# Optimization experiments

Hardware: AMD Instinct MI355X
Metric: run time of the kernel (lower is better)

The kernel has to match this reference:

```python
import jax, jax.numpy as jnp
import numpy as np

N = 50000          # nodes
E = 1_600_000      # edges (avg degree 32)
IN = 128           # in_channels
H = 64             # hidden_channels = middle_channel
OUT = 40           # out_channels
ALPHA = 0.8
NO_GRAD_STEPS = 3  # iter_nums = (4, 1) -> 3 no-grad + 1 grad step
GRAD_STEPS = 1
LN_EPS = 1e-5


def setup_inputs() -> dict:
    key = jax.random.key(0)
    ks = jax.random.split(key, 8)
    x = jax.random.normal(ks[0], (N, IN), jnp.float32)
    edge_index = jax.random.randint(ks[1], (2, E), 0, N, dtype=jnp.int64)
    # per-node symmetric-normalization factor, strictly positive (deg^-1/2-like)
    norm_factor = jax.random.uniform(ks[2], (N, 1), jnp.float32, 0.1, 1.0)
    kaiming = lambda k, shape, fan_in: jax.random.normal(k, shape, jnp.float32) * np.float32(np.sqrt(2.0 / fan_in))
    We = kaiming(ks[3], (H, IN), IN)      # extractor weight
    be = jnp.zeros((H,), jnp.float32)
    W = kaiming(ks[4], (H, H), H)         # Implicit_Func.W (no bias)
    U = kaiming(ks[5], (H, H), H)         # Implicit_Func.U
    bU = jnp.zeros((H,), jnp.float32)
    gamma = jnp.ones((H,), jnp.float32)   # LayerNorm affine
    beta = jnp.zeros((H,), jnp.float32)
    Wlast = jax.random.normal(ks[6], (OUT, H), jnp.float32) * np.float32(np.sqrt(2.0 / (H + OUT)))  # xavier
    blast = jnp.zeros((OUT,), jnp.float32)
    return dict(x=x, edge_index=edge_index, norm_factor=norm_factor,
                We=We, be=be, W=W, U=U, bU=bU, gamma=gamma, beta=beta,
                Wlast=Wlast, blast=blast)


def _layernorm(m, gamma, beta):
    mu = jnp.mean(m, axis=-1, keepdims=True)
    var = jnp.mean((m - mu) ** 2, axis=-1, keepdims=True)
    return gamma * (m - mu) * jax.lax.rsqrt(var + LN_EPS) + beta


def _step(z, xU, nf, row, col, W, gamma, beta):
    # WzUx = norm_factor * (W z + degree * U x)   (xU precomputed as degree*(Ux+b))
    h = nf * (z @ W.T + xU)                       # [N, H]
    m = jnp.tanh(h[row] - h[col])                 # gather-diff + act, [E, H]
    m = _layernorm(m, gamma, beta)
    # scatter_add back to nodes with norm weighting
    a = (jax.ops.segment_sum(m * nf[row], row, num_segments=N)
         - jax.ops.segment_sum(m * nf[col], col, num_segments=N))  # [N, H]
    new_z = -(a @ W)                              # F.linear(a, W.t()) = a @ W
    return ALPHA * new_z + (1.0 - ALPHA) * z


def reference(x, edge_index, norm_factor, We, be, W, U, bU, gamma, beta, Wlast, blast):
    row, col = edge_index[0], edge_index[1]
    xh = x @ We.T + be                            # extractor, [N, H]
    degree = 1.0 / norm_factor
    degree = jnp.where(jnp.isinf(degree), 0.0, degree)
    xU = degree * (xh @ U.T + bU)                 # constant across iterations
    z = jnp.zeros_like(xh)
    for _ in range(NO_GRAD_STEPS):
        z = _step(z, xU, norm_factor, row, col, W, gamma, beta)
    z = jax.lax.stop_gradient(z)
    for _ in range(GRAD_STEPS):
        z = _step(z, xU, norm_factor, row, col, W, gamma, beta)
    z = norm_factor * z + xh                      # rescale + residual
    return z @ Wlast.T + blast                    # linear head, [N, OUT]
```

## Files before the change

kernel.cpp:

```cpp
#include <hip/hip_runtime.h>
#include <hip/hip_bf16.h>

#define NN   50000
#define EE   1600000
#define INC  128
#define HH   64
#define OUTC 40
#define ALPHA 0.8f
#define LN_EPS 1e-5f
#define NB_SCAN 196
#define KTANH 2.8853900817779268f

typedef int v4i_t __attribute__((ext_vector_type(4)));
typedef _Float16 h8 __attribute__((ext_vector_type(8)));
typedef float f32x4 __attribute__((ext_vector_type(4)));

__device__ float llvm_amdgcn_raw_buffer_load_fp32(v4i_t srsrc, int voffset,
                                                  int soffset, int glc_slc)
    __asm("llvm.amdgcn.raw.buffer.load.f32");

__device__ __forceinline__ float rl63(float x) {
    return __int_as_float(__builtin_amdgcn_readlane(__float_as_int(x), 63));
}
#define RLF(X, L) __int_as_float(__builtin_amdgcn_readlane(__float_as_int(X), (L)))

__device__ __forceinline__ float fast_tanh_pre(float xs) {
    float e = __builtin_amdgcn_exp2f(xs);
    float u = __builtin_amdgcn_rcpf(1.0f + e);
    return __builtin_fmaf(-2.0f, u, 1.0f);
}

struct TileAcc { float a0, a1, a2, a3, sc; };

template <bool GUARD>
__device__ __forceinline__ void tile16(
        TileAcc& A, float hn, int nrem,
        float h0, float h1, float h2, float h3,
        float h4, float h5, float h6, float h7,
        float h8v, float h9, float h10, float h11,
        float h12, float h13, float h14, float h15,
        _Float16* tb, int wt, int wlow, int roff0, int roff1, h8 ones) {
    float d0 = fast_tanh_pre(hn - h0);
    float d1 = fast_tanh_pre(hn - h1);
    float d2 = fast_tanh_pre(hn - h2);
    float d3 = fast_tanh_pre(hn - h3);
    float d4 = fast_tanh_pre(hn - h4);
    float d5 = fast_tanh_pre(hn - h5);
    float d6 = fast_tanh_pre(hn - h6);
    float d7 = fast_tanh_pre(hn - h7);
    float d8 = fast_tanh_pre(hn - h8v);
    float d9 = fast_tanh_pre(hn - h9);
    float d10 = fast_tanh_pre(hn - h10);
    float d11 = fast_tanh_pre(hn - h11);
    float d12 = fast_tanh_pre(hn - h12);
    float d13 = fast_tanh_pre(hn - h13);
    float d14 = fast_tanh_pre(hn - h14);
    float d15 = fast_tanh_pre(hn - h15);
    if (GUARD) {
        if (!(0 < nrem))  d0 = 0.f;
        if (!(1 < nrem))  d1 = 0.f;
        if (!(2 < nrem))  d2 = 0.f;
        if (!(3 < nrem))  d3 = 0.f;
        if (!(4 < nrem))  d4 = 0.f;
        if (!(5 < nrem))  d5 = 0.f;
        if (!(6 < nrem))  d6 = 0.f;
        if (!(7 < nrem))  d7 = 0.f;
        if (!(8 < nrem))  d8 = 0.f;
        if (!(9 < nrem))  d9 = 0.f;
        if (!(10 < nrem)) d10 = 0.f;
        if (!(11 < nrem)) d11 = 0.f;
        if (!(12 < nrem)) d12 = 0.f;
        if (!(13 < nrem)) d13 = 0.f;
        if (!(14 < nrem)) d14 = 0.f;
        if (!(15 < nrem)) d15 = 0.f;
    }
#define WRT(E, D)                                                             \
    {                                                                         \
        int ix = ((wt ^ ((E) & 7)) << 3) + wlow + ((E) << 6);                 \
        tb[ix] = (_Float16)(D);                                               \
        tb[ix + 1024] = (_Float16)((D) * (D));                                \
    }
    WRT(0, d0)   WRT(1, d1)   WRT(2, d2)   WRT(3, d3)
    WRT(4, d4)   WRT(5, d5)   WRT(6, d6)   WRT(7, d7)
    WRT(8, d8)   WRT(9, d9)   WRT(10, d10) WRT(11, d11)
    WRT(12, d12) WRT(13, d13) WRT(14, d14) WRT(15, d15)
#undef WRT
    h8 a0 = *(const h8*)(tb + roff0);
    h8 a1 = *(const h8*)(tb + roff1);
    h8 q0 = *(const h8*)(tb + 1024 + roff0);
    h8 q1 = *(const h8*)(tb + 1024 + roff1);
    f32x4 s1 = {0.f, 0.f, 0.f, 0.f}, s2 = {0.f, 0.f, 0.f, 0.f};
    s1 = __builtin_amdgcn_mfma_f32_16x16x32_f16(a0, ones, s1, 0, 0, 0);
    s1 = __builtin_amdgcn_mfma_f32_16x16x32_f16(a1, ones, s1, 0, 0, 0);
    s2 = __builtin_amdgcn_mfma_f32_16x16x32_f16(q0, ones, s2, 0, 0, 0);
    s2 = __builtin_amdgcn_mfma_f32_16x16x32_f16(q1, ones, s2, 0, 0, 0);
    float mu0 = s1[0] * 0.015625f;
    float mu1 = s1[1] * 0.015625f;
    float mu2 = s1[2] * 0.015625f;
    float mu3 = s1[3] * 0.015625f;
    float v0 = __builtin_fmaf(s2[0], 0.015625f, __builtin_fmaf(-mu0, mu0, LN_EPS));
    float v1 = __builtin_fmaf(s2[1], 0.015625f, __builtin_fmaf(-mu1, mu1, LN_EPS));
    float v2 = __builtin_fmaf(s2[2], 0.015625f, __builtin_fmaf(-mu2, mu2, LN_EPS));
    float v3 = __builtin_fmaf(s2[3], 0.015625f, __builtin_fmaf(-mu3, mu3, LN_EPS));
    float rs0 = __frsqrt_rn(v0);
    float rs1 = __frsqrt_rn(v1);
    float rs2 = __frsqrt_rn(v2);
    float rs3 = __frsqrt_rn(v3);
    float cs = __builtin_fmaf(rs0, mu0,
               __builtin_fmaf(rs1, mu1,
               __builtin_fmaf(rs2, mu2, rs3 * mu3)));
    asm volatile(
        "s_nop 1\n\t"
        "v_add_f32_dpp %0, %0, %0 row_bcast:15 row_mask:0xa bank_mask:0xf bound_ctrl:0\n\t"
        "s_nop 1\n\t"
        "v_add_f32_dpp %0, %0, %0 row_bcast:31 row_mask:0xc bank_mask:0xf bound_ctrl:0"
        : "+v"(cs));
    A.sc += rl63(cs);
    A.a0 = __builtin_fmaf(RLF(rs0, 0), d0, A.a0);
    A.a1 = __builtin_fmaf(RLF(rs1, 0), d1, A.a1);
    A.a2 = __builtin_fmaf(RLF(rs2, 0), d2, A.a2);
    A.a3 = __builtin_fmaf(RLF(rs3, 0), d3, A.a3);
    A.a0 = __builtin_fmaf(RLF(rs0, 16), d4, A.a0);
    A.a1 = __builtin_fmaf(RLF(rs1, 16), d5, A.a1);
    A.a2 = __builtin_fmaf(RLF(rs2, 16), d6, A.a2);
    A.a3 = __builtin_fmaf(RLF(rs3, 16), d7, A.a3);
    A.a0 = __builtin_fmaf(RLF(rs0, 32), d8, A.a0);
    A.a1 = __builtin_fmaf(RLF(rs1, 32), d9, A.a1);
    A.a2 = __builtin_fmaf(RLF(rs2, 32), d10, A.a2);
    A.a3 = __builtin_fmaf(RLF(rs3, 32), d11, A.a3);
    A.a0 = __builtin_fmaf(RLF(rs0, 48), d12, A.a0);
    A.a1 = __builtin_fmaf(RLF(rs1, 48), d13, A.a1);
    A.a2 = __builtin_fmaf(RLF(rs2, 48), d14, A.a2);
    A.a3 = __builtin_fmaf(RLF(rs3, 48), d15, A.a3);
}

__global__ __launch_bounds__(256) void csr_count(const int* __restrict__ ei,
                                                 int* __restrict__ cnt,
                                                 unsigned short* __restrict__ rank16) {
    int i = blockIdx.x * 256 + threadIdx.x;
    if (i >= 2 * EE) return;
    int r = atomicAdd(&cnt[ei[i]], 1);
    rank16[i] = (unsigned short)r;
}

__global__ __launch_bounds__(256) void scanA(const int* __restrict__ cnt,
                                             int* __restrict__ offs,
                                             int* __restrict__ bsum) {
    __shared__ int tmp[256];
    int i = blockIdx.x * 256 + threadIdx.x;
    int v = (i < NN) ? cnt[i] : 0;
    tmp[threadIdx.x] = v;
    __syncthreads();
    int acc = v;
    for (int d = 1; d < 256; d <<= 1) {
        int t = (threadIdx.x >= d) ? tmp[threadIdx.x - d] : 0;
        __syncthreads();
        acc += t;
        tmp[threadIdx.x] = acc;
        __syncthreads();
    }
    if (i < NN) offs[i] = acc - v;
    if (threadIdx.x == 255) bsum[blockIdx.x] = acc;
}

__global__ __launch_bounds__(256) void scanB(int* __restrict__ bsum) {
    __shared__ int tmp[256];
    int v = (threadIdx.x < NB_SCAN) ? bsum[threadIdx.x] : 0;
    tmp[threadIdx.x] = v;
    __syncthreads();
    int acc = v;
    for (int d = 1; d < 256; d <<= 1) {
        int t = (threadIdx.x >= d) ? tmp[threadIdx.x - d] : 0;
        __syncthreads();
        acc += t;
        tmp[threadIdx.x] = acc;
        __syncthreads();
    }
    if (threadIdx.x < NB_SCAN) bsum[threadIdx.x] = acc - v;
}

__global__ __launch_bounds__(256) void scanC(int* __restrict__ offs,
                                             const int* __restrict__ bsum) {
    int i = blockIdx.x * 256 + threadIdx.x;
    if (i < NN) offs[i] += bsum[blockIdx.x];
}

__global__ __launch_bounds__(256) void csr_fill(const int* __restrict__ ei,
                                                const int* __restrict__ offs,
                                                const unsigned short* __restrict__ rank16,
                                                int* __restrict__ adj) {
    int i = blockIdx.x * 256 + threadIdx.x;
    if (i >= 2 * EE) return;
    int node  = ei[i];
    int role  = (i >= EE) ? 1 : 0;
    int other = role ? ei[i - EE] : ei[i + EE];
    adj[offs[node] + (int)rank16[i]] =
        (int)(((unsigned)other << 8) | ((unsigned)role << 31));
}

__global__ __launch_bounds__(256) void make_G(const float* __restrict__ W,
                                              float* __restrict__ G) {
    __shared__ float Ws[64 * 64];
    for (int t = threadIdx.x; t < 64 * 64; t += 256) Ws[t] = W[t];
    __syncthreads();
    for (int t = threadIdx.x; t < 64 * 64; t += 256) {
        int i = t >> 6, j = t & 63;
        float acc = 0.f;
#pragma unroll 8
        for (int k = 0; k < 64; ++k) acc += Ws[i * 64 + k] * Ws[j * 64 + k];
        G[t] = acc;
    }
}

__global__ __launch_bounds__(256) void extractor(
        const float* __restrict__ x, const float* __restrict__ nf,
        const float* __restrict__ We, const float* __restrict__ be,
        const float* __restrict__ U,  const float* __restrict__ bU,
        float* __restrict__ xh, float* __restrict__ xU, float* __restrict__ h0) {
    __shared__ float WeT[INC * HH];
    __shared__ float UT[HH * HH];
    __shared__ float beS[HH], bUS[HH];
    __shared__ float xs[4][INC];
    __shared__ float xhs[4][HH];

    for (int t = threadIdx.x; t < INC * HH; t += 256) {
        int j = t >> 7, k = t & 127;
        WeT[k * 64 + j] = We[t];
    }
    for (int t = threadIdx.x; t < HH * HH; t += 256) {
        int j = t >> 6, k = t & 63;
        UT[k * 64 + j] = U[t];
    }
    if (threadIdx.x < 64) { beS[threadIdx.x] = be[threadIdx.x]; bUS[threadIdx.x] = bU[threadIdx.x]; }
    __syncthreads();

    int lane = threadIdx.x & 63;
    int wv   = threadIdx.x >> 6;

    for (int n0 = blockIdx.x * 4; n0 < NN; n0 += gridDim.x * 4) {
        int n = n0 + wv;
        bool valid = n < NN;
        if (valid) {
            xs[wv][lane]      = x[(size_t)n * INC + lane];
            xs[wv][lane + 64] = x[(size_t)n * INC + lane + 64];
        }
        __syncthreads();
        float acc = beS[lane];
        if (valid) {
#pragma unroll 8
            for (int k = 0; k < INC; ++k) acc += xs[wv][k] * WeT[k * 64 + lane];
            xh[n * 64 + lane] = acc;
            xhs[wv][lane] = acc;
        }
        __syncthreads();
        if (valid) {
            float acc2 = bUS[lane];
#pragma unroll 8
            for (int k = 0; k < HH; ++k) acc2 += xhs[wv][k] * UT[k * 64 + lane];
            h0[n * 64 + lane] = KTANH * acc2;
            xU[n * 64 + lane] = acc2 / nf[n];
        }
        __syncthreads();
    }
}

#define HV(P) P##0, P##1, P##2, P##3, P##4, P##5, P##6, P##7,                 \
              P##8, P##9, P##10, P##11, P##12, P##13, P##14, P##15

#define G16(P, EV, J)                                                          \
    do {                                                                       \
        P##0  = GATH(RL(EV, (J) + 0));  P##1  = GATH(RL(EV, (J) + 1));         \
        P##2  = GATH(RL(EV, (J) + 2));  P##3  = GATH(RL(EV, (J) + 3));         \
        P##4  = GATH(RL(EV, (J) + 4));  P##5  = GATH(RL(EV, (J) + 5));         \
        P##6  = GATH(RL(EV, (J) + 6));  P##7  = GATH(RL(EV, (J) + 7));         \
        P##8  = GATH(RL(EV, (J) + 8));  P##9  = GATH(RL(EV, (J) + 9));         \
        P##10 = GATH(RL(EV, (J) + 10)); P##11 = GATH(RL(EV, (J) + 11));        \
        P##12 = GATH(RL(EV, (J) + 12)); P##13 = GATH(RL(EV, (J) + 13));        \
        P##14 = GATH(RL(EV, (J) + 14)); P##15 = GATH(RL(EV, (J) + 15));        \
    } while (0)

#define NEXTPREF(P)                                                            \
    do {                                                                       \
        if (morechunk)      { G16(P, evB, 0); }                                \
        else if (morenode)  { G16(P, evN, 0); }                                \
    } while (0)

__global__ __launch_bounds__(256) void fused_step(
        const int* __restrict__ adj, const int* __restrict__ offs,
        const int* __restrict__ cnt,
        const float* __restrict__ hcur, float* __restrict__ hnxt,
        const float* __restrict__ nf, const float* __restrict__ gamma,
        const float* __restrict__ beta, const float* __restrict__ Gm,
        const float* __restrict__ xU,
        float* __restrict__ y, float* __restrict__ s, int first, int last) {
    __shared__ float Gs[64 * 64];
    __shared__ __align__(16) _Float16 dt[4][2048];
    for (int t = threadIdx.x; t < 64 * 64; t += 256) Gs[t] = Gm[t];
    __syncthreads();

    const int lane = threadIdx.x & 63, wv = threadIdx.x >> 6;
    const float g = gamma[lane], b = beta[lane];

    v4i_t hsr;
    {
        unsigned long long up = (unsigned long long)(uintptr_t)hcur;
        hsr.x = (int)(unsigned)(up & 0xffffffffull);
        hsr.y = (int)(unsigned)(up >> 32);
        hsr.z = NN * HH * 4;
        hsr.w = 0x00020000;
    }
    const int lane4 = lane << 2;
#define GATH(e) llvm_amdgcn_raw_buffer_load_fp32(hsr, lane4, (e) & 0x00ffff00, 0)
#define RL(v, i) __builtin_amdgcn_readlane((v), (i))

    _Float16* tb = &dt[wv][0];
    const int wt   = lane >> 3;
    const int wlow = lane & 7;
    const int re = lane & 15, rg = lane >> 4, rc = lane & 7;
    const int roff0 = re * 64 + ((rg) ^ rc) * 8;
    const int roff1 = re * 64 + ((4 + rg) ^ rc) * 8;
    const h8 ones = {(_Float16)1.f, (_Float16)1.f, (_Float16)1.f, (_Float16)1.f,
                     (_Float16)1.f, (_Float16)1.f, (_Float16)1.f, (_Float16)1.f};

    const int NW = 2048 * 4;
    int n = blockIdx.x * 4 + wv;
    int base = __builtin_amdgcn_readfirstlane(offs[n]);
    int deg  = __builtin_amdgcn_readfirstlane(cnt[n]);
    int ev   = adj[base + lane];
    float hn = hcur[(size_t)n * 64 + lane];
    float hA0, hA1, hA2, hA3, hA4, hA5, hA6, hA7;
    float hA8, hA9, hA10, hA11, hA12, hA13, hA14, hA15;
    float hB0, hB1, hB2, hB3, hB4, hB5, hB6, hB7;
    float hB8, hB9, hB10, hB11, hB12, hB13, hB14, hB15;
    G16(hA, ev, 0);

    for (;;) {
        const int nxt = n + NW;
        const bool morenode = nxt < NN;
        int baseN = 0, degN = 0, evN = 0;
        float hnN = 0.f;
        if (morenode) {
            baseN = __builtin_amdgcn_readfirstlane(offs[nxt]);
            degN  = __builtin_amdgcn_readfirstlane(cnt[nxt]);
            evN   = adj[baseN + lane];
            hnN   = hcur[(size_t)nxt * 64 + lane];
        }
        TileAcc A = {0.f, 0.f, 0.f, 0.f, 0.f};
        int sigma = 0;

        if (deg > 0) {
            int cbase = 0;
            for (;;) {
                int nE = deg - cbase;
                if (nE > 64) nE = 64;
                const bool morechunk = (cbase + 64 < deg);
                int evB = 0;
                if (morechunk) evB = adj[base + cbase + 64 + lane];
                unsigned long long bal = __ballot(ev < 0);
                unsigned long long msk =
                    (nE >= 64) ? ~0ull : ((1ull << nE) - 1ull);
                sigma += nE - 2 * (int)__builtin_popcountll(bal & msk);

                if (nE == 64) {
                    G16(hB, ev, 16);
                    tile16<false>(A, hn, 0, HV(hA), tb, wt, wlow, roff0, roff1, ones);
                    G16(hA, ev, 32);
                    tile16<false>(A, hn, 0, HV(hB), tb, wt, wlow, roff0, roff1, ones);
                    G16(hB, ev, 48);
                    tile16<false>(A, hn, 0, HV(hA), tb, wt, wlow, roff0, roff1, ones);
                    NEXTPREF(hA);
                    tile16<false>(A, hn, 0, HV(hB), tb, wt, wlow, roff0, roff1, ones);
                } else {
                    const int nt = (nE + 15) >> 4;
                    if (nt > 1) { G16(hB, ev, 16); } else { NEXTPREF(hB); }
                    tile16<true>(A, hn, nE, HV(hA), tb, wt, wlow, roff0, roff1, ones);
                    if (nt > 1) {
                        if (nt > 2) { G16(hA, ev, 32); } else { NEXTPREF(hA); }
                        tile16<true>(A, hn, nE - 16, HV(hB), tb, wt, wlow, roff0, roff1, ones);
                        if (nt > 2) {
                            if (nt > 3) { G16(hB, ev, 48); } else { NEXTPREF(hB); }
                            tile16<true>(A, hn, nE - 32, HV(hA), tb, wt, wlow, roff0, roff1, ones);
                            if (nt > 3) {
                                NEXTPREF(hA);
                                tile16<true>(A, hn, nE - 48, HV(hB), tb, wt, wlow, roff0, roff1, ones);
                            }
                        }
                    }
                    if (nt & 1) {
                        hA0 = hB0;  hA1 = hB1;  hA2 = hB2;  hA3 = hB3;
                        hA4 = hB4;  hA5 = hB5;  hA6 = hB6;  hA7 = hB7;
                        hA8 = hB8;  hA9 = hB9;  hA10 = hB10; hA11 = hB11;
                        hA12 = hB12; hA13 = hB13; hA14 = hB14; hA15 = hB15;
                    }
                }
                if (!morechunk) break;
                ev = evB;
                cbase += 64;
            }
        } else {
            if (morenode) { G16(hA, evN, 0); }
        }

        const float accM = ((A.a0 + A.a1) + (A.a2 + A.a3)) - A.sc;
        const float nfn = nf[n];
        const float av  = nfn * __builtin_fmaf(g, accM, b * (float)sigma);

        float p = 0.f;
        const int avi = __float_as_int(av);
#pragma unroll
        for (int k = 0; k < 64; ++k) {
            float ak = __int_as_float(RL(avi, k));
            p = __builtin_fmaf(ak, Gs[k * 64 + lane], p);
        }

        float yprev = 0.f, sprev = 0.f;
        if (!first) {
            yprev = y[n * 64 + lane];
            sprev = s[n * 64 + lane];
        }
        const float yv = -ALPHA * p + (1.0f - ALPHA) * yprev;
        y[n * 64 + lane] = yv;
        s[n * 64 + lane] = (1.0f - ALPHA) * sprev + av;
        if (!last) hnxt[n * 64 + lane] = KTANH * (nfn * (yv + xU[n * 64 + lane]));

        if (!morenode) break;
        n = nxt; base = baseN; deg = degN;
        ev = evN; hn = hnN;
    }
#undef GATH
#undef RL
}

__global__ __launch_bounds__(256) void final_out(
        const float* __restrict__ s, const float* __restrict__ xh,
        const float* __restrict__ nf, const float* __restrict__ W,
        const float* __restrict__ Wlast, const float* __restrict__ blast,
        float* __restrict__ out) {
    __shared__ float Ws[64 * 64];
    __shared__ float WlT[64 * OUTC];
    __shared__ float blS[OUTC];
    __shared__ float ss[4][64];
    __shared__ float zfs[4][64];
    for (int t = threadIdx.x; t < 64 * 64; t += 256) Ws[t] = W[t];
    for (int t = threadIdx.x; t < OUTC * 64; t += 256) {
        int o = t >> 6, j = t & 63;
        WlT[j * OUTC + o] = Wlast[t];
    }
    if (threadIdx.x < OUTC) blS[threadIdx.x] = blast[threadIdx.x];
    __syncthreads();
    int lane = threadIdx.x & 63, wv = threadIdx.x >> 6;
    for (int n0 = blockIdx.x * 4; n0 < NN; n0 += gridDim.x * 4) {
        int n = n0 + wv;
        if (n < NN) ss[wv][lane] = s[n * 64 + lane];
        __syncthreads();
        if (n < NN) {
            float z = 0.f;
#pragma unroll 8
            for (int k = 0; k < 64; ++k) z += ss[wv][k] * Ws[k * 64 + lane];
            z *= -ALPHA;
            zfs[wv][lane] = nf[n] * z + xh[n * 64 + lane];
        }
        __syncthreads();
        if (n < NN && lane < OUTC) {
            float acc = blS[lane];
#pragma unroll 8
            for (int j = 0; j < 64; ++j) acc += zfs[wv][j] * WlT[j * OUTC + lane];
            out[n * OUTC + lane] = acc;
        }
        __syncthreads();
    }
}

extern "C" void kernel_launch(void* const* d_in, const int* in_sizes, int n_in,
                              void* d_out, int out_size, void* d_ws, size_t ws_size,
                              hipStream_t stream) {
    const float* x     = (const float*)d_in[0];
    const int*   ei    = (const int*)  d_in[1];
    const float* nf    = (const float*)d_in[2];
    const float* We    = (const float*)d_in[3];
    const float* be    = (const float*)d_in[4];
    const float* W     = (const float*)d_in[5];
    const float* U     = (const float*)d_in[6];
    const float* bU    = (const float*)d_in[7];
    const float* gamma = (const float*)d_in[8];
    const float* beta  = (const float*)d_in[9];
    const float* Wlast = (const float*)d_in[10];
    const float* blast = (const float*)d_in[11];
    float* out = (float*)d_out;

    char* ws = (char*)d_ws;
    size_t off = 0;
    const size_t NH = (size_t)NN * HH * sizeof(float);
    int*   adj    = (int*)(ws + off);            off += (size_t)2 * EE * sizeof(int);
    unsigned short* rank16 = (unsigned short*)(ws + off);
                                                 off += (size_t)2 * EE * sizeof(unsigned short);
    int*   offs   = (int*)(ws + off);            off += (size_t)NN * sizeof(int);
    int*   cnt    = (int*)(ws + off);            off += (size_t)NN * sizeof(int);
    int*   bsum   = (int*)(ws + off);            off += 256 * sizeof(int);
    float* xh     = (float*)(ws + off);          off += NH;
    float* xU     = (float*)(ws + off);          off += NH;
    float* h0     = (float*)(ws + off);          off += NH;
    float* h1     = (float*)(ws + off);          off += NH;
    float* y      = (float*)(ws + off);          off += NH;
    float* s      = (float*)(ws + off);          off += NH;
    float* G      = (float*)(ws + off);          off += (size_t)HH * HH * sizeof(float);

    hipMemsetAsync(cnt, 0, (size_t)NN * sizeof(int), stream);

    csr_count<<<(2 * EE + 255) / 256, 256, 0, stream>>>(ei, cnt, rank16);
    scanA<<<NB_SCAN, 256, 0, stream>>>(cnt, offs, bsum);
    scanB<<<1, 256, 0, stream>>>(bsum);
    scanC<<<NB_SCAN, 256, 0, stream>>>(offs, bsum);
    csr_fill<<<(2 * EE + 255) / 256, 256, 0, stream>>>(ei, offs, rank16, adj);

    make_G<<<1, 256, 0, stream>>>(W, G);
    extractor<<<2048, 256, 0, stream>>>(x, nf, We, be, U, bU, xh, xU, h0);

    float* hc = h0;
    float* hn = h1;
    for (int t = 0; t < 4; ++t) {
        fused_step<<<2048, 256, 0, stream>>>(adj, offs, cnt, hc, hn, nf,
                                             gamma, beta, G, xU, y, s,
                                             t == 0, t == 3);
        float* tmp = hc; hc = hn; hn = tmp;
    }
    final_out<<<2048, 256, 0, stream>>>(s, xh, nf, W, Wlast, blast, out);
}
```

Before: 1.072 ms.

## Use transpose LDS reads for LayerNorm tiles and precompute edge-role sign counts

Result: faster. 991.8 us (-7.5%).

```diff
diff --git a/kernel.cpp b/kernel.cpp
--- a/kernel.cpp
+++ b/kernel.cpp
@@ -13,7 +13,10 @@
 
 typedef int v4i_t __attribute__((ext_vector_type(4)));
 typedef _Float16 h8 __attribute__((ext_vector_type(8)));
+typedef __fp16 hv2 __attribute__((ext_vector_type(2)));
 typedef float f32x4 __attribute__((ext_vector_type(4)));
+typedef int i32x2 __attribute__((ext_vector_type(2)));
+typedef int i32x4 __attribute__((ext_vector_type(4)));
 
 __device__ float llvm_amdgcn_raw_buffer_load_fp32(v4i_t srsrc, int voffset,
                                                   int soffset, int glc_slc)
@@ -30,7 +33,16 @@
     return __builtin_fmaf(-2.0f, u, 1.0f);
 }
 
+__device__ __forceinline__ h8 mk8(i32x2 a, i32x2 b) {
+    i32x4 t = {a.x, a.y, b.x, b.y};
+    return __builtin_bit_cast(h8, t);
+}
+
 struct TileAcc { float a0, a1, a2, a3, sc; };
+
+#define TRRD(D, OFF)                                                           \
+    asm volatile("ds_read_b64_tr_b16 %0, %1 offset:" OFF                       \
+                 : "=v"(D) : "v"(trv))
 
 template <bool GUARD>
 __device__ __forceinline__ void tile16(
@@ -39,7 +51,7 @@
         float h4, float h5, float h6, float h7,
         float h8v, float h9, float h10, float h11,
         float h12, float h13, float h14, float h15,
-        _Float16* tb, int wt, int wlow, int roff0, int roff1, h8 ones) {
+        char* wp, int trv, h8 ones) {
     float d0 = fast_tanh_pre(hn - h0);
     float d1 = fast_tanh_pre(hn - h1);
     float d2 = fast_tanh_pre(hn - h2);
@@ -74,26 +86,41 @@
         if (!(14 < nrem)) d14 = 0.f;
         if (!(15 < nrem)) d15 = 0.f;
     }
-#define WRT(E, D)                                                             \
-    {                                                                         \
-        int ix = ((wt ^ ((E) & 7)) << 3) + wlow + ((E) << 6);                 \
-        tb[ix] = (_Float16)(D);                                               \
-        tb[ix + 1024] = (_Float16)((D) * (D));                                \
-    }
-    WRT(0, d0)   WRT(1, d1)   WRT(2, d2)   WRT(3, d3)
-    WRT(4, d4)   WRT(5, d5)   WRT(6, d6)   WRT(7, d7)
-    WRT(8, d8)   WRT(9, d9)   WRT(10, d10) WRT(11, d11)
-    WRT(12, d12) WRT(13, d13) WRT(14, d14) WRT(15, d15)
-#undef WRT
-    h8 a0 = *(const h8*)(tb + roff0);
-    h8 a1 = *(const h8*)(tb + roff1);
-    h8 q0 = *(const h8*)(tb + 1024 + roff0);
-    h8 q1 = *(const h8*)(tb + 1024 + roff1);
+    hv2 p0 = __builtin_amdgcn_cvt_pkrtz(d0, d1);
+    hv2 p1 = __builtin_amdgcn_cvt_pkrtz(d2, d3);
+    hv2 p2 = __builtin_amdgcn_cvt_pkrtz(d4, d5);
+    hv2 p3 = __builtin_amdgcn_cvt_pkrtz(d6, d7);
+    hv2 p4 = __builtin_amdgcn_cvt_pkrtz(d8, d9);
+    hv2 p5 = __builtin_amdgcn_cvt_pkrtz(d10, d11);
+    hv2 p6 = __builtin_amdgcn_cvt_pkrtz(d12, d13);
+    hv2 p7 = __builtin_amdgcn_cvt_pkrtz(d14, d15);
+    hv2 q0 = p0 * p0, q1 = p1 * p1, q2 = p2 * p2, q3 = p3 * p3;
+    hv2 q4 = p4 * p4, q5 = p5 * p5, q6 = p6 * p6, q7 = p7 * p7;
+#define BC(X) __builtin_bit_cast(int, X)
+    i32x4 wA = {BC(p0), BC(p1), BC(p2), BC(p3)};
+    i32x4 wB = {BC(p4), BC(p5), BC(p6), BC(p7)};
+    i32x4 wC = {BC(q0), BC(q1), BC(q2), BC(q3)};
+    i32x4 wD = {BC(q4), BC(q5), BC(q6), BC(q7)};
+#undef BC
+    *(i32x4*)(wp)        = wA;
+    *(i32x4*)(wp + 16)   = wB;
+    *(i32x4*)(wp + 2048) = wC;
+    *(i32x4*)(wp + 2064) = wD;
+    asm volatile("" ::: "memory");
+    i32x2 r0, r1, r2, r3, r4, r5, r6, r7;
+    TRRD(r0, "0");    TRRD(r1, "128");
+    TRRD(r2, "1024"); TRRD(r3, "1152");
+    TRRD(r4, "2048"); TRRD(r5, "2176");
+    TRRD(r6, "3072"); TRRD(r7, "3200");
+    asm volatile("s_waitcnt lgkmcnt(0)" ::: "memory");
+    __builtin_amdgcn_sched_barrier(0);
+    h8 a0 = mk8(r0, r1), a1 = mk8(r2, r3);
+    h8 b0 = mk8(r4, r5), b1 = mk8(r6, r7);
     f32x4 s1 = {0.f, 0.f, 0.f, 0.f}, s2 = {0.f, 0.f, 0.f, 0.f};
     s1 = __builtin_amdgcn_mfma_f32_16x16x32_f16(a0, ones, s1, 0, 0, 0);
     s1 = __builtin_amdgcn_mfma_f32_16x16x32_f16(a1, ones, s1, 0, 0, 0);
-    s2 = __builtin_amdgcn_mfma_f32_16x16x32_f16(q0, ones, s2, 0, 0, 0);
-    s2 = __builtin_amdgcn_mfma_f32_16x16x32_f16(q1, ones, s2, 0, 0, 0);
+    s2 = __builtin_amdgcn_mfma_f32_16x16x32_f16(b0, ones, s2, 0, 0, 0);
+    s2 = __builtin_amdgcn_mfma_f32_16x16x32_f16(b1, ones, s2, 0, 0, 0);
     float mu0 = s1[0] * 0.015625f;
     float mu1 = s1[1] * 0.015625f;
     float mu2 = s1[2] * 0.015625f;
@@ -106,16 +133,9 @@
     float rs1 = __frsqrt_rn(v1);
     float rs2 = __frsqrt_rn(v2);
     float rs3 = __frsqrt_rn(v3);
-    float cs = __builtin_fmaf(rs0, mu0,
-               __builtin_fmaf(rs1, mu1,
-               __builtin_fmaf(rs2, mu2, rs3 * mu3)));
-    asm volatile(
-        "s_nop 1\n\t"
-        "v_add_f32_dpp %0, %0, %0 row_bcast:15 row_mask:0xa bank_mask:0xf bound_ctrl:0\n\t"
-        "s_nop 1\n\t"
-        "v_add_f32_dpp %0, %0, %0 row_bcast:31 row_mask:0xc bank_mask:0xf bound_ctrl:0"
-        : "+v"(cs));
-    A.sc += rl63(cs);
+    A.sc += __builtin_fmaf(rs0, mu0,
+            __builtin_fmaf(rs1, mu1,
+            __builtin_fmaf(rs2, mu2, rs3 * mu3)));
     A.a0 = __builtin_fmaf(RLF(rs0, 0), d0, A.a0);
     A.a1 = __builtin_fmaf(RLF(rs1, 0), d1, A.a1);
     A.a2 = __builtin_fmaf(RLF(rs2, 0), d2, A.a2);
@@ -139,7 +159,8 @@
                                                  unsigned short* __restrict__ rank16) {
     int i = blockIdx.x * 256 + threadIdx.x;
     if (i >= 2 * EE) return;
-    int r = atomicAdd(&cnt[ei[i]], 1);
+    int add = (i >= EE) ? 0x10001 : 1;
+    int r = atomicAdd(&cnt[ei[i]], add);
     rank16[i] = (unsigned short)r;
 }
 
@@ -148,7 +169,7 @@
                                              int* __restrict__ bsum) {
     __shared__ int tmp[256];
     int i = blockIdx.x * 256 + threadIdx.x;
-    int v = (i < NN) ? cnt[i] : 0;
+    int v = (i < NN) ? (cnt[i] & 0xffff) : 0;
     tmp[threadIdx.x] = v;
     __syncthreads();
     int acc = v;
@@ -192,10 +213,8 @@
     int i = blockIdx.x * 256 + threadIdx.x;
     if (i >= 2 * EE) return;
     int node  = ei[i];
-    int role  = (i >= EE) ? 1 : 0;
-    int other = role ? ei[i - EE] : ei[i + EE];
-    adj[offs[node] + (int)rank16[i]] =
-        (int)(((unsigned)other << 8) | ((unsigned)role << 31));
+    int other = (i >= EE) ? ei[i - EE] : ei[i + EE];
+    adj[offs[node] + (int)rank16[i]] = other << 8;
 }
 
 __global__ __launch_bounds__(256) void make_G(const float* __restrict__ W,
@@ -310,22 +329,22 @@
         hsr.w = 0x00020000;
     }
     const int lane4 = lane << 2;
-#define GATH(e) llvm_amdgcn_raw_buffer_load_fp32(hsr, lane4, (e) & 0x00ffff00, 0)
+#define GATH(e) llvm_amdgcn_raw_buffer_load_fp32(hsr, lane4, (e), 0)
 #define RL(v, i) __builtin_amdgcn_readlane((v), (i))
 
     _Float16* tb = &dt[wv][0];
-    const int wt   = lane >> 3;
-    const int wlow = lane & 7;
-    const int re = lane & 15, rg = lane >> 4, rc = lane & 7;
-    const int roff0 = re * 64 + ((rg) ^ rc) * 8;
-    const int roff1 = re * 64 + ((4 + rg) ^ rc) * 8;
+    char* wp = (char*)tb + lane * 32;
+    const unsigned tbb = (unsigned)(uintptr_t)tb;
+    const int trv = (int)(tbb + ((lane >> 4) << 8) + ((lane & 15) << 3));
     const h8 ones = {(_Float16)1.f, (_Float16)1.f, (_Float16)1.f, (_Float16)1.f,
                      (_Float16)1.f, (_Float16)1.f, (_Float16)1.f, (_Float16)1.f};
 
     const int NW = 2048 * 4;
     int n = blockIdx.x * 4 + wv;
+    int cP   = __builtin_amdgcn_readfirstlane(cnt[n]);
     int base = __builtin_amdgcn_readfirstlane(offs[n]);
-    int deg  = __builtin_amdgcn_readfirstlane(cnt[n]);
+    int deg  = cP & 0xffff;
+    int sgm  = deg - 2 * ((int)((unsigned)cP >> 16));
     int ev   = adj[base + lane];
     float hn = hcur[(size_t)n * 64 + lane];
     float hA0, hA1, hA2, hA3, hA4, hA5, hA6, hA7;
@@ -337,16 +356,15 @@
     for (;;) {
         const int nxt = n + NW;
         const bool morenode = nxt < NN;
-        int baseN = 0, degN = 0, evN = 0;
+        int baseN = 0, cN = 0, evN = 0;
         float hnN = 0.f;
         if (morenode) {
             baseN = __builtin_amdgcn_readfirstlane(offs[nxt]);
-            degN  = __builtin_amdgcn_readfirstlane(cnt[nxt]);
+            cN    = __builtin_amdgcn_readfirstlane(cnt[nxt]);
             evN   = adj[baseN + lane];
             hnN   = hcur[(size_t)nxt * 64 + lane];
         }
         TileAcc A = {0.f, 0.f, 0.f, 0.f, 0.f};
-        int sigma = 0;
 
         if (deg > 0) {
             int cbase = 0;
@@ -356,33 +374,29 @@
                 const bool morechunk = (cbase + 64 < deg);
                 int evB = 0;
                 if (morechunk) evB = adj[base + cbase + 64 + lane];
-                unsigned long long bal = __ballot(ev < 0);
-                unsigned long long msk =
-                    (nE >= 64) ? ~0ull : ((1ull << nE) - 1ull);
-                sigma += nE - 2 * (int)__builtin_popcountll(bal & msk);
 
                 if (nE == 64) {
                     G16(hB, ev, 16);
-                    tile16<false>(A, hn, 0, HV(hA), tb, wt, wlow, roff0, roff1, ones);
+                    tile16<false>(A, hn, 0, HV(hA), wp, trv, ones);
                     G16(hA, ev, 32);
-                    tile16<false>(A, hn, 0, HV(hB), tb, wt, wlow, roff0, roff1, ones);
+                    tile16<false>(A, hn, 0, HV(hB), wp, trv, ones);
                     G16(hB, ev, 48);
-                    tile16<false>(A, hn, 0, HV(hA), tb, wt, wlow, roff0, roff1, ones);
+                    tile16<false>(A, hn, 0, HV(hA), wp, trv, ones);
                     NEXTPREF(hA);
-                    tile16<false>(A, hn, 0, HV(hB), tb, wt, wlow, roff0, roff1, ones);
+                    tile16<false>(A, hn, 0, HV(hB), wp, trv, ones);
                 } else {
                     const int nt = (nE + 15) >> 4;
                     if (nt > 1) { G16(hB, ev, 16); } else { NEXTPREF(hB); }
-                    tile16<true>(A, hn, nE, HV(hA), tb, wt, wlow, roff0, roff1, ones);
+                    tile16<true>(A, hn, nE, HV(hA), wp, trv, ones);
                     if (nt > 1) {
                         if (nt > 2) { G16(hA, ev, 32); } else { NEXTPREF(hA); }
-                        tile16<true>(A, hn, nE - 16, HV(hB), tb, wt, wlow, roff0, roff1, ones);
+                        tile16<true>(A, hn, nE - 16, HV(hB), wp, trv, ones);
                         if (nt > 2) {
                             if (nt > 3) { G16(hB, ev, 48); } else { NEXTPREF(hB); }
-                            tile16<true>(A, hn, nE - 32, HV(hA), tb, wt, wlow, roff0, roff1, ones);
+                            tile16<true>(A, hn, nE - 32, HV(hA), wp, trv, ones);
                             if (nt > 3) {
                                 NEXTPREF(hA);
-                                tile16<true>(A, hn, nE - 48, HV(hB), tb, wt, wlow, roff0, roff1, ones);
+                                tile16<true>(A, hn, nE - 48, HV(hB), wp, trv, ones);
                             }
                         }
                     }
@@ -401,9 +415,16 @@
             if (morenode) { G16(hA, evN, 0); }
         }
 
-        const float accM = ((A.a0 + A.a1) + (A.a2 + A.a3)) - A.sc;
+        float scp = A.sc;
+        asm volatile(
+            "s_nop 1\n\t"
+            "v_add_f32_dpp %0, %0, %0 row_bcast:15 row_mask:0xa bank_mask:0xf bound_ctrl:0\n\t"
+            "s_nop 1\n\t"
+            "v_add_f32_dpp %0, %0, %0 row_bcast:31 row_mask:0xc bank_mask:0xf bound_ctrl:0"
+            : "+v"(scp));
+        const float accM = ((A.a0 + A.a1) + (A.a2 + A.a3)) - rl63(scp);
         const float nfn = nf[n];
-        const float av  = nfn * __builtin_fmaf(g, accM, b * (float)sigma);
+        const float av  = nfn * __builtin_fmaf(g, accM, b * (float)sgm);
 
         float p = 0.f;
         const int avi = __float_as_int(av);
@@ -424,7 +445,9 @@
         if (!last) hnxt[n * 64 + lane] = KTANH * (nfn * (yv + xU[n * 64 + lane]));
 
         if (!morenode) break;
-        n = nxt; base = baseN; deg = degN;
+        n = nxt; base = baseN;
+        deg = cN & 0xffff;
+        sgm = deg - 2 * ((int)((unsigned)cN >> 16));
         ev = evN; hn = hnN;
     }
 #undef GATH
@@ -491,7 +514,7 @@
     char* ws = (char*)d_ws;
     size_t off = 0;
     const size_t NH = (size_t)NN * HH * sizeof(float);
-    int*   adj    = (int*)(ws + off);            off += (size_t)2 * EE * sizeof(int);
+    int*   adj    = (int*)(ws + off);            off += (size_t)2 * EE * sizeof(int) + 256;
     unsigned short* rank16 = (unsigned short*)(ws + off);
                                                  off += (size_t)2 * EE * sizeof(unsigned short);
     int*   offs   = (int*)(ws + off);            off += (size_t)NN * sizeof(int);
@@ -505,7 +528,7 @@
     float* s      = (float*)(ws + off);          off += NH;
     float* G      = (float*)(ws + off);          off += (size_t)HH * HH * sizeof(float);
 
-    hipMemsetAsync(cnt, 0, (size_t)NN * sizeof(int), stream);
+    (void)hipMemsetAsync(cnt, 0, (size_t)NN * sizeof(int), stream);
 
     csr_count<<<(2 * EE + 255) / 256, 256, 0, stream>>>(ei, cnt, rank16);
     scanA<<<NB_SCAN, 256, 0, stream>>>(cnt, offs, bsum);
```
